# Performance work log

Hardware: AMD Instinct MI355X
Metric: run time of the kernel (lower is better)

The kernel has to match this reference:

```python
import jax, jax.numpy as jnp
import numpy as np

KS = 3
N = KS * KS
LN_EPS = 1e-5


def conv2d(x, w, stride=1, pad=0):
    return jax.lax.conv_general_dilated(
        x, w, (stride, stride), [(pad, pad), (pad, pad)],
        dimension_numbers=('NCHW', 'OIHW', 'NCHW'))


def layer_norm(x, g, b):
    mu = jnp.mean(x, axis=-1, keepdims=True)
    var = jnp.mean(jnp.square(x - mu), axis=-1, keepdims=True)
    return (x - mu) * jax.lax.rsqrt(var + LN_EPS) * g + b


def l2norm(x):
    n = jnp.sqrt(jnp.sum(jnp.square(x), axis=-1, keepdims=True))
    return x / jnp.maximum(n, 1e-12)


def deform_conv(x, w_p, b_p, w_d):
    # canonical DeformConv2d (kernel 3, pad 1, stride 1, no modulation)
    B, C, H, W = x.shape
    off = conv2d(x, w_p, stride=1, pad=1) + b_p[None, :, None, None]  # [B,2N,H,W]
    xp = jnp.pad(x, ((0, 0), (0, 0), (1, 1), (1, 1)))
    Hp, Wp = H + 2, W + 2
    pn = jnp.stack(jnp.meshgrid(jnp.arange(-1, 2), jnp.arange(-1, 2), indexing='ij'), 0)
    pn = pn.reshape(2, N).astype(x.dtype)  # kernel offsets, row-major (dx,dy)
    p0x = jnp.arange(1, H + 1, dtype=x.dtype)
    p0y = jnp.arange(1, W + 1, dtype=x.dtype)
    # sampling coords, [B,H,W,N]
    px = off[:, :N].transpose(0, 2, 3, 1) + p0x[None, :, None, None] + pn[0][None, None, None, :]
    py = off[:, N:].transpose(0, 2, 3, 1) + p0y[None, None, :, None] + pn[1][None, None, None, :]
    fx = jnp.floor(px)
    fy = jnp.floor(py)
    qlx = jnp.clip(fx, 0, Hp - 1)
    qly = jnp.clip(fy, 0, Wp - 1)
    qrx = jnp.clip(fx + 1, 0, Hp - 1)
    qry = jnp.clip(fy + 1, 0, Wp - 1)
    pxc = jnp.clip(px, 0, Hp - 1)
    pyc = jnp.clip(py, 0, Wp - 1)
    g_lt = (1 + (qlx - pxc)) * (1 + (qly - pyc))
    g_rb = (1 - (qrx - pxc)) * (1 - (qry - pyc))
    g_lb = (1 + (qlx - pxc)) * (1 - (qry - pyc))
    g_rt = (1 - (qrx - pxc)) * (1 + (qly - pyc))
    xf = xp.reshape(B, C, Hp * Wp)

    def gat(ix, iy):
        idx = (ix.astype(jnp.int32) * Wp + iy.astype(jnp.int32)).reshape(B, 1, -1)
        g = jnp.take_along_axis(xf, jnp.broadcast_to(idx, (B, C, idx.shape[-1])), axis=2)
        return g.reshape(B, C, H, W, N)

    xo = (g_lt[:, None] * gat(qlx, qly) + g_rb[:, None] * gat(qrx, qry)
          + g_lb[:, None] * gat(qlx, qry) + g_rt[:, None] * gat(qrx, qly))
    # [B,C,H,W,N] -> [B,C,H*ks,W*ks] (row = h*ks+kr, col = w*ks+kc)
    xo = xo.reshape(B, C, H, W, KS, KS).transpose(0, 1, 2, 4, 3, 5).reshape(B, C, H * KS, W * KS)
    return conv2d(xo, w_d, stride=KS, pad=0)


def setup_inputs() -> dict:
    key = jax.random.key(0)
    ks = jax.random.split(key, 8)
    B, C, H, W, heads = 4, 192, 64, 64, 6
    hid = 4 * C
    return {
        'x': jax.random.normal(ks[0], (B, C, H, W), dtype=jnp.float32),
        'gamma1': jnp.ones((C,), jnp.float32),
        'beta1': jnp.zeros((C,), jnp.float32),
        'gamma2': jnp.ones((C,), jnp.float32),
        'beta2': jnp.zeros((C,), jnp.float32),
        'temperature': jnp.ones((heads, 1, 1), jnp.float32),
        'w_qkv': jax.random.normal(ks[1], (3 * C, C), jnp.float32) * 0.02,
        'w_proj': jax.random.normal(ks[2], (C, C), jnp.float32) * 0.02,
        'w_p': jax.random.normal(ks[3], (2 * N, C, KS, KS), jnp.float32) * 0.01,
        'b_p': jnp.zeros((2 * N,), jnp.float32),
        'w_d': jax.random.normal(ks[4], (C, C, KS, KS), jnp.float32) * 0.02,
        'w_fc1': jax.random.normal(ks[5], (C, hid), jnp.float32) * 0.02,
        'b_fc1': jnp.zeros((hid,), jnp.float32),
        'w_fc2': jax.random.normal(ks[6], (hid, C), jnp.float32) * 0.02,
        'b_fc2': jnp.zeros((C,), jnp.float32),
    }


def reference(x, gamma1, beta1, gamma2, beta2, temperature, w_qkv, w_proj,
              w_p, b_p, w_d, w_fc1, b_fc1, w_fc2, b_fc2):
    B, C, H, W = x.shape
    heads = temperature.shape[0]
    xs = x.reshape(B, C, H * W).transpose(0, 2, 1)  # [B,HW,C]
    shortcut = xs
    xn = layer_norm(xs, gamma1, beta1).transpose(0, 2, 1).reshape(B, C, H, W)
    # SSA: deformable-conv query + channel attention over C
    q = deform_conv(xn, w_p, b_p, w_d)
    qkv = jnp.einsum('bchw,oc->bohw', xn, w_qkv)
    k_spe, v_spe = qkv[:, C:2 * C], qkv[:, 2 * C:]

    def split(t):
        return t.reshape(B, heads, C // heads, H * W)

    qh = split(q)
    kh = l2norm(split(k_spe))
    vh = l2norm(split(v_spe))
    attn = jnp.einsum('bhcn,bhdn->bhcd', qh, kh) * temperature[None]
    attn = jax.nn.softmax(attn, axis=-1)
    out = jnp.einsum('bhcd,bhdn->bhcn', attn, vh).reshape(B, C, H, W)
    out = jnp.einsum('bchw,oc->bohw', out, w_proj)
    xs2 = shortcut + out.reshape(B, C, H * W).transpose(0, 2, 1)
    h1 = layer_norm(xs2, gamma2, beta2)
    m = jax.nn.gelu(h1 @ w_fc1 + b_fc1, approximate=False) @ w_fc2 + b_fc2
    xs3 = xs2 + m
    return xs3.transpose(0, 2, 1).reshape(B, C, H, W)
```

## Files before the change

### kernel.cpp

```cpp
#include <hip/hip_runtime.h>
#include <math.h>

typedef unsigned short u16;
typedef unsigned int u32;
typedef short s16x8 __attribute__((ext_vector_type(8)));
typedef float f32x4 __attribute__((ext_vector_type(4)));

#define AS1 __attribute__((address_space(1)))
#define AS3 __attribute__((address_space(3)))

__device__ __forceinline__ float bf2f(u16 u) {
    union { u32 i; float f; } v; v.i = ((u32)u) << 16; return v.f;
}
__device__ __forceinline__ u16 f2bf(float f) {
    union { float f; u32 i; } v; v.f = f;
    u32 r = v.i + 0x7fffu + ((v.i >> 16) & 1u);
    return (u16)(r >> 16);
}
__device__ __forceinline__ void gll16(const u16* g, u16* l) {
    __builtin_amdgcn_global_load_lds((const AS1 u32*)g, (AS3 u32*)l, 16, 0, 0);
}

__global__ void prep_kernel(const float* __restrict__ wd, const float* __restrict__ wqkv,
                            const float* __restrict__ wfc1, const float* __restrict__ wfc2,
                            const float* __restrict__ wp,
                            u16* __restrict__ wdT, u16* __restrict__ wkvT,
                            u16* __restrict__ wf1T, u16* __restrict__ wf2T,
                            u16* __restrict__ wpT)
{
    int i = blockIdx.x * 256 + threadIdx.x;
    if (i < 331776) {
        int o = i / 1728, r = i % 1728;
        int p = r / 192, c = r % 192;
        int cs = c ^ ((o & 7) << 3);
        wdT[(p * 192 + o) * 192 + cs] = f2bf(wd[(o * 192 + c) * 9 + p]);
    }
    if (i < 73728) {
        int o = i / 192, c = i % 192;
        wkvT[i] = f2bf(wqkv[(192 + o) * 192 + c]);
    }
    if (i < 147456) {
        int n = i / 192, c = i % 192;
        wf1T[i] = f2bf(wfc1[c * 768 + n]);
        int n2 = i / 768, hh = i % 768;
        wf2T[i] = f2bf(wfc2[hh * 192 + n2]);
    }
    if (i < 31104) {
        int n = i / 1728, r = i % 1728;
        int p = r / 192, c = r % 192;
        wpT[i] = f2bf(wp[(n * 192 + c) * 9 + p]);
    } else if (i < 55296) {
        wpT[i] = 0;
    }
}

__global__ __launch_bounds__(256) void ln1_kernel(const float* __restrict__ x,
                                                  const float* __restrict__ g,
                                                  const float* __restrict__ be,
                                                  u16* __restrict__ xn)
{
    __shared__ float red0[256], red1[256];
    __shared__ float mu_s[64], rs_s[64];
    __shared__ float xt[64 * 193];
    __shared__ u16 tile[64 * 194];
    int t = threadIdx.x, tl = t & 63, cg = t >> 6;
    int m0 = blockIdx.x * 64;
    int b = m0 >> 12, hw0 = m0 & 4095;
    const float* xb = x + (size_t)b * 786432 + hw0 + tl;
    float s = 0.f, s2 = 0.f;
    for (int cc = cg; cc < 192; cc += 4) {
        float v = xb[cc * 4096];
        xt[tl * 193 + cc] = v;
        s += v; s2 += v * v;
    }
    red0[t] = s; red1[t] = s2;
    __syncthreads();
    if (t < 64) {
        float a = red0[t] + red0[64 + t] + red0[128 + t] + red0[192 + t];
        float q = red1[t] + red1[64 + t] + red1[128 + t] + red1[192 + t];
        float mu = a * (1.f / 192.f);
        float var = q * (1.f / 192.f) - mu * mu;
        mu_s[t] = mu; rs_s[t] = rsqrtf(var + 1e-5f);
    }
    __syncthreads();
    float mu = mu_s[tl], rs = rs_s[tl];
    for (int cc = cg; cc < 192; cc += 4) {
        float v = (xt[tl * 193 + cc] - mu) * rs * g[cc] + be[cc];
        tile[tl * 194 + cc] = f2bf(v);
    }
    __syncthreads();
    u32* dst = (u32*)(xn + (size_t)m0 * 192);
    for (int i = t; i < 64 * 96; i += 256) {
        int r = i / 96, c2 = i % 96;
        dst[i] = *(const u32*)&tile[r * 194 + c2 * 2];
    }
}

__global__ __launch_bounds__(256) void offconv_kernel(const u16* __restrict__ xn,
                                                      const u16* __restrict__ wpT,
                                                      const float* __restrict__ bp,
                                                      float* __restrict__ off)
{
    __shared__ u16 As[64 * 200];
    __shared__ u16 Bs[32 * 200];
    int bh = blockIdx.x;
    int b = bh >> 6, h = bh & 63;
    int t = threadIdx.x;
    int lane = t & 63, wv = t >> 6;
    f32x4 acc[2];
#pragma unroll
    for (int j = 0; j < 2; j++) { acc[j][0] = 0.f; acc[j][1] = 0.f; acc[j][2] = 0.f; acc[j][3] = 0.f; }
    int r = t >> 2, cq = (t & 3) * 48;
    for (int p = 0; p < 9; p++) {
        int dh = p / 3 - 1, dw = p % 3 - 1;
        int hr = h + dh, wr = r + dw;
        bool valid = (hr >= 0) && (hr < 64) && (wr >= 0) && (wr < 64);
        const u16* src = xn + ((size_t)(b * 4096 + hr * 64 + wr)) * 192 + cq;
#pragma unroll
        for (int j = 0; j < 6; j++) {
            s16x8 v = {0, 0, 0, 0, 0, 0, 0, 0};
            if (valid) v = *(const s16x8*)(src + j * 8);
            *(s16x8*)&As[r * 200 + cq + j * 8] = v;
        }
#pragma unroll
        for (int i = 0; i < 3; i++) {
            int q = t + i * 256;
            int n = q / 24, c8 = q % 24;
            *(s16x8*)&Bs[n * 200 + c8 * 8] =
                *(const s16x8*)(wpT + n * 1728 + p * 192 + c8 * 8);
        }
        __syncthreads();
#pragma unroll
        for (int kc = 0; kc < 6; kc++) {
            s16x8 af = *(const s16x8*)&As[(wv * 16 + (lane & 15)) * 200 + kc * 32 + (lane >> 4) * 8];
            s16x8 b0 = *(const s16x8*)&Bs[(lane & 15) * 200 + kc * 32 + (lane >> 4) * 8];
            s16x8 b1 = *(const s16x8*)&Bs[(16 + (lane & 15)) * 200 + kc * 32 + (lane >> 4) * 8];
            acc[0] = __builtin_amdgcn_mfma_f32_16x16x32_bf16(af, b0, acc[0], 0, 0, 0);
            acc[1] = __builtin_amdgcn_mfma_f32_16x16x32_bf16(af, b1, acc[1], 0, 0, 0);
        }
        __syncthreads();
    }
    int col = lane & 15;
    int wbase = wv * 16 + (lane >> 4) * 4;
#pragma unroll
    for (int j = 0; j < 2; j++) {
        int n = j * 16 + col;
        if (n < 18) {
            float bb = bp[n];
#pragma unroll
            for (int rr = 0; rr < 4; rr++) {
                int w = wbase + rr;
                off[((size_t)(b * 4096 + h * 64 + w)) * 18 + n] = acc[j][rr] + bb;
            }
        }
    }
}

__global__ __launch_bounds__(512, 2) void gemm_deform(const u16* __restrict__ xn,
                                                      const float* __restrict__ off,
                                                      const u16* __restrict__ wdT,
                                                      u16* __restrict__ qt)
{
    __shared__ u16 As[64 * 200];
    __shared__ u16 Bs[192 * 192];
    __shared__ int sidx[64][9][4];
    __shared__ float swt[64][9][4];
    int t = threadIdx.x, lane = t & 63, wv = t >> 6;
    int wm = wv & 1, wn = wv >> 1;
    int m0 = blockIdx.x * 64;
    int b = m0 >> 12;
    for (int i = t; i < 576; i += 512) {
        int mi = i / 9, p = i % 9;
        int m = m0 + mi;
        int hw = m & 4095;
        int h = hw >> 6, w = hw & 63;
        float ox = off[(size_t)m * 18 + p];
        float oy = off[(size_t)m * 18 + 9 + p];
        float px = ox + (float)(h + 1) + (float)(p / 3 - 1);
        float py = oy + (float)(w + 1) + (float)(p % 3 - 1);
        float fx = floorf(px), fy = floorf(py);
        float qlx = fminf(fmaxf(fx, 0.f), 65.f);
        float qly = fminf(fmaxf(fy, 0.f), 65.f);
        float qrx = fminf(fmaxf(fx + 1.f, 0.f), 65.f);
        float qry = fminf(fmaxf(fy + 1.f, 0.f), 65.f);
        float pxc = fminf(fmaxf(px, 0.f), 65.f);
        float pyc = fminf(fmaxf(py, 0.f), 65.f);
        float gxl = 1.f + (qlx - pxc), gxr = 1.f - (qrx - pxc);
        float gyl = 1.f + (qly - pyc), gyr = 1.f - (qry - pyc);
        int xl = (int)qlx, xr = (int)qrx, yl = (int)qly, yr = (int)qry;
        int cx[4] = {xl, xr, xl, xr};
        int cy[4] = {yl, yr, yr, yl};
        float cw[4] = {gxl * gyl, gxr * gyr, gxl * gyr, gxr * gyl};
#pragma unroll
        for (int k = 0; k < 4; k++) {
            bool ok = (cx[k] >= 1) && (cx[k] <= 64) && (cy[k] >= 1) && (cy[k] <= 64);
            sidx[mi][p][k] = ok ? (b * 4096 + (cx[k] - 1) * 64 + (cy[k] - 1)) * 192 : 0;
            swt[mi][p][k] = ok ? cw[k] : 0.f;
        }
    }
    __syncthreads();
    f32x4 acc[2][3];
#pragma unroll
    for (int i = 0; i < 2; i++)
#pragma unroll
        for (int j = 0; j < 3; j++) {
            acc[i][j][0] = 0.f; acc[i][j][1] = 0.f; acc[i][j][2] = 0.f; acc[i][j][3] = 0.f;
        }
    int mi = t >> 3, ch = (t & 7) * 24;
    int orow[3], oxr[3];
#pragma unroll
    for (int j = 0; j < 3; j++) {
        int o = wn * 48 + j * 16 + (lane & 15);
        orow[j] = o * 192;
        oxr[j] = (o & 7) << 3;
    }
    int kb0 = (lane >> 4) * 8;

    {
        const u16* bsrc = wdT;
#pragma unroll
        for (int i2 = 0; i2 < 9; i2++) {
            int jc = wv + 8 * i2;
            gll16(bsrc + jc * 512 + lane * 8, Bs + jc * 512);
        }
        const int*   si = sidx[mi][0];
        const float* sw = swt[mi][0];
        s16x8 pc[4][3];
#pragma unroll
        for (int k = 0; k < 4; k++)
#pragma unroll
            for (int s = 0; s < 3; s++)
                pc[k][s] = *(const s16x8*)(xn + si[k] + ch + s * 8);
        float v[24];
#pragma unroll
        for (int j = 0; j < 24; j++) v[j] = 0.f;
#pragma unroll
        for (int k = 0; k < 4; k++) {
            float wt = sw[k];
#pragma unroll
            for (int j = 0; j < 24; j++) v[j] += wt * bf2f((u16)pc[k][j >> 3][j & 7]);
        }
#pragma unroll
        for (int s = 0; s < 3; s++) {
            s16x8 ov;
#pragma unroll
            for (int e = 0; e < 8; e++) ov[e] = (short)f2bf(v[s * 8 + e]);
            *(s16x8*)&As[mi * 200 + ch + s * 8] = ov;
        }
        asm volatile("s_waitcnt vmcnt(0)" ::: "memory");
        __syncthreads();
    }

    for (int p = 0; p < 9; p++) {
        s16x8 nc[4][3];
        if (p < 8) {
            const int* si = sidx[mi][p + 1];
#pragma unroll
            for (int k = 0; k < 4; k++)
#pragma unroll
                for (int s = 0; s < 3; s++)
                    nc[k][s] = *(const s16x8*)(xn + si[k] + ch + s * 8);
        }
#pragma unroll
        for (int kk = 0; kk < 6; kk++) {
            int kb = kk * 32 + kb0;
            s16x8 af[2], bfr[3];
#pragma unroll
            for (int i = 0; i < 2; i++)
                af[i] = *(const s16x8*)&As[(wm * 32 + i * 16 + (lane & 15)) * 200 + kb];
#pragma unroll
            for (int j = 0; j < 3; j++)
                bfr[j] = *(const s16x8*)&Bs[orow[j] + (kb ^ oxr[j])];
#pragma unroll
            for (int i = 0; i < 2; i++)
#pragma unroll
                for (int j = 0; j < 3; j++)
                    acc[i][j] = __builtin_amdgcn_mfma_f32_16x16x32_bf16(af[i], bfr[j], acc[i][j], 0, 0, 0);
        }
        if (p < 8) {
            __syncthreads();
            const u16* bsrc = wdT + (size_t)(p + 1) * 36864;
#pragma unroll
            for (int i2 = 0; i2 < 9; i2++) {
                int jc = wv + 8 * i2;
                gll16(bsrc + jc * 512 + lane * 8, Bs + jc * 512);
            }
            const float* sw = swt[mi][p + 1];
            float v[24];
#pragma unroll
            for (int j = 0; j < 24; j++) v[j] = 0.f;
#pragma unroll
            for (int k = 0; k < 4; k++) {
                float wt = sw[k];
#pragma unroll
                for (int j = 0; j < 24; j++) v[j] += wt * bf2f((u16)nc[k][j >> 3][j & 7]);
            }
#pragma unroll
            for (int s = 0; s < 3; s++) {
                s16x8 ov;
#pragma unroll
                for (int e = 0; e < 8; e++) ov[e] = (short)f2bf(v[s * 8 + e]);
                *(s16x8*)&As[mi * 200 + ch + s * 8] = ov;
            }
            asm volatile("s_waitcnt vmcnt(0)" ::: "memory");
            __syncthreads();
        }
    }
    int col = lane & 15;
#pragma unroll
    for (int i = 0; i < 2; i++)
#pragma unroll
        for (int j = 0; j < 3; j++) {
            int mm = m0 + wm * 32 + i * 16 + (lane >> 4) * 4;
            int nn = wn * 48 + j * 16 + col;
#pragma unroll
            for (int r = 0; r < 4; r++)
                qt[(size_t)(mm + r) * 192 + nn] = f2bf(acc[i][j][r]);
        }
}

template<int BM, int BN, int WM, int WN, int EP>
__global__ __launch_bounds__((BM / WM) * (BN / WN) * 64)
void gemm_bt(const u16* __restrict__ A, int lda,
             const u16* __restrict__ B, int ldb, int bstride,
             void* __restrict__ out, int ldc,
             const float* __restrict__ ex1, int K,
             const float* __restrict__ ex2,
             const float* __restrict__ exg, const float* __restrict__ exb,
             void* __restrict__ out2)
{
    constexpr int BK = 32;
    constexpr int WAVES_M = BM / WM, WAVES_N = BN / WN, NW = WAVES_M * WAVES_N;
    constexpr int TM = WM / 16, TN = WN / 16;
    constexpr int NLA = BM / 16, NLB = BN / 16;
    __shared__ u16 As[BM * BK];
    __shared__ u16 Bs[BN * BK];
    int tid = threadIdx.x;
    int lane = tid & 63, wv = tid >> 6;
    int wm = wv % WAVES_M, wn = wv / WAVES_M;
    int m0 = blockIdx.x * BM, n0 = blockIdx.y * BN;
    const u16* Bp = B + (size_t)(m0 >> 12) * bstride;
    f32x4 acc[TM][TN];
#pragma unroll
    for (int i = 0; i < TM; i++)
#pragma unroll
        for (int j = 0; j < TN; j++) {
            acc[i][j][0] = 0.f; acc[i][j][1] = 0.f; acc[i][j][2] = 0.f; acc[i][j][3] = 0.f;
        }
    int arow_l = lane >> 2;
    int acol_l = (lane & 3) * 8;
    for (int k0 = 0; k0 < K; k0 += BK) {
#pragma unroll 1
        for (int j = wv; j < NLA + NLB; j += NW) {
            if (j < NLA) {
                int row = j * 16 + arow_l;
                gll16(A + (size_t)(m0 + row) * lda + k0 + acol_l, As + j * 512);
            } else {
                int row = (j - NLA) * 16 + arow_l;
                gll16(Bp + (size_t)(n0 + row) * ldb + k0 + acol_l, Bs + (j - NLA) * 512);
            }
        }
        asm volatile("s_waitcnt vmcnt(0)" ::: "memory");
        __syncthreads();
        s16x8 af[TM], bfr[TN];
#pragma unroll
        for (int i = 0; i < TM; i++)
            af[i] = *(const s16x8*)&As[(wm * WM + i * 16 + (lane & 15)) * BK + (lane >> 4) * 8];
#pragma unroll
        for (int j = 0; j < TN; j++)
            bfr[j] = *(const s16x8*)&Bs[(wn * WN + j * 16 + (lane & 15)) * BK + (lane >> 4) * 8];
#pragma unroll
        for (int i = 0; i < TM; i++)
#pragma unroll
            for (int j = 0; j < TN; j++)
                acc[i][j] = __builtin_amdgcn_mfma_f32_16x16x32_bf16(af[i], bfr[j], acc[i][j], 0, 0, 0);
        __syncthreads();
    }
    int col = lane & 15;
    int rg = lane >> 4;
    if constexpr (EP == 0) {
        u16* o = (u16*)out;
#pragma unroll
        for (int i = 0; i < TM; i++)
#pragma unroll
            for (int j = 0; j < TN; j++) {
                int mm = m0 + wm * WM + i * 16 + rg * 4;
                int nn = n0 + wn * WN + j * 16 + col;
#pragma unroll
                for (int r = 0; r < 4; r++) o[(size_t)(mm + r) * ldc + nn] = f2bf(acc[i][j][r]);
            }
    } else if constexpr (EP == 2) {
        u16* o = (u16*)out;
#pragma unroll
        for (int i = 0; i < TM; i++)
#pragma unroll
            for (int j = 0; j < TN; j++) {
                int mm = m0 + wm * WM + i * 16 + rg * 4;
                int nn = n0 + wn * WN + j * 16 + col;
                float bb = ex1[nn];
#pragma unroll
                for (int r = 0; r < 4; r++) {
                    float v = acc[i][j][r] + bb;
                    o[(size_t)(mm + r) * ldc + nn] = f2bf(0.5f * v * (1.f + erff(v * 0.70710678118654752f)));
                }
            }
    } else if constexpr (EP == 4) {
        __shared__ float lnA[BM][2];
        __shared__ float lnB[BM][2];
        float v[TM][TN][4];
        float sr[TM][4], sq[TM][4];
#pragma unroll
        for (int i = 0; i < TM; i++)
#pragma unroll
            for (int r = 0; r < 4; r++) { sr[i][r] = 0.f; sq[i][r] = 0.f; }
#pragma unroll
        for (int i = 0; i < TM; i++) {
            int mm = m0 + wm * WM + i * 16 + rg * 4;
#pragma unroll
            for (int j = 0; j < TN; j++) {
                int nn = n0 + wn * WN + j * 16 + col;
                const float* xr = ex1 + (size_t)(mm >> 12) * 786432 + (size_t)nn * 4096 + (mm & 4095);
#pragma unroll
                for (int r = 0; r < 4; r++) {
                    float vv = acc[i][j][r] + xr[r];
                    v[i][j][r] = vv;
                    sr[i][r] += vv; sq[i][r] += vv * vv;
                }
            }
        }
#pragma unroll
        for (int i = 0; i < TM; i++)
#pragma unroll
            for (int r = 0; r < 4; r++)
#pragma unroll
                for (int sh = 1; sh < 16; sh <<= 1) {
                    sr[i][r] += __shfl_xor(sr[i][r], sh);
                    sq[i][r] += __shfl_xor(sq[i][r], sh);
                }
        if (col == 0) {
#pragma unroll
            for (int i = 0; i < TM; i++)
#pragma unroll
                for (int r = 0; r < 4; r++) {
                    int row = wm * WM + i * 16 + rg * 4 + r;
                    lnA[row][wn] = sr[i][r];
                    lnB[row][wn] = sq[i][r];
                }
        }
        __syncthreads();
        float* oxs = (float*)out;
        u16* oh = (u16*)out2;
#pragma unroll
        for (int i = 0; i < TM; i++) {
            int mm = m0 + wm * WM + i * 16 + rg * 4;
#pragma unroll
            for (int r = 0; r < 4; r++) {
                int row = wm * WM + i * 16 + rg * 4 + r;
                float tot = lnA[row][0] + lnA[row][1];
                float tq  = lnB[row][0] + lnB[row][1];
                float mu = tot * (1.f / 192.f);
                float var = tq * (1.f / 192.f) - mu * mu;
                float rstd = rsqrtf(var + 1e-5f);
#pragma unroll
                for (int j = 0; j < TN; j++) {
                    int nn = n0 + wn * WN + j * 16 + col;
                    float vv = v[i][j][r];
                    oxs[(size_t)(mm + r) * ldc + nn] = vv;
                    oh[(size_t)(mm + r) * ldc + nn] = f2bf((vv - mu) * rstd * exg[nn] + exb[nn]);
                }
            }
        }
    } else if constexpr (EP == 5) {
        float* o = (float*)out;
#pragma unroll
        for (int i = 0; i < TM; i++)
#pragma unroll
            for (int j = 0; j < TN; j++) {
                int mm = m0 + wm * WM + i * 16 + rg * 4;
                int nn = n0 + wn * WN + j * 16 + col;
                float bb = ex1[nn];
                size_t obase = (size_t)(mm >> 12) * 786432 + (size_t)nn * 4096;
#pragma unroll
                for (int r = 0; r < 4; r++) {
                    float vv = acc[i][j][r] + bb + ex2[(size_t)(mm + r) * ldc + nn];
                    o[obase + ((mm + r) & 4095)] = vv;
                }
            }
    } else if constexpr (EP == 6) {
        u16* o = (u16*)out;
        float* nrm = (float*)out2;
        int bI = m0 >> 12;
#pragma unroll
        for (int j = 0; j < TN; j++) {
            float s = 0.f;
#pragma unroll
            for (int i = 0; i < TM; i++) {
                int mm = m0 + wm * WM + i * 16 + rg * 4;
                int nn = n0 + wn * WN + j * 16 + col;
#pragma unroll
                for (int r = 0; r < 4; r++) {
                    u16 hb = f2bf(acc[i][j][r]);
                    o[(size_t)(mm + r) * ldc + nn] = hb;
                    float fv = bf2f(hb);
                    s += fv * fv;
                }
            }
            s += __shfl_xor(s, 16);
            s += __shfl_xor(s, 32);
            if (rg == 0) {
                int nn = n0 + wn * WN + j * 16 + col;
                atomicAdd(&nrm[bI * 384 + nn], s);
            }
        }
    }
}

__global__ __launch_bounds__(64) void attnp_kernel(const u16* __restrict__ qt,
                                                   const u16* __restrict__ kvt,
                                                   float* __restrict__ raw)
{
    __shared__ float qT[32 * 69];
    __shared__ float kT[32 * 69];
    int ch = blockIdx.x, h = blockIdx.y, b = blockIdx.z;
    int t = threadIdx.x;
    size_t base = (size_t)(b * 4096 + ch * 64);
    for (int e = t; e < 2048; e += 64) {
        int r = e >> 5, c = e & 31;
        qT[c * 69 + r] = bf2f(qt[(base + r) * 192 + h * 32 + c]);
        kT[c * 69 + r] = bf2f(kvt[(base + r) * 384 + h * 32 + c]);
    }
    __syncthreads();
    int tc = t >> 3, td = t & 7;
    int c0 = tc * 4, d0 = td * 4;
    float acc[4][4] = {};
    for (int r = 0; r < 64; r++) {
        float qv[4], kv4[4];
#pragma unroll
        for (int u = 0; u < 4; u++) { qv[u] = qT[(c0 + u) * 69 + r]; kv4[u] = kT[(d0 + u) * 69 + r]; }
#pragma unroll
        for (int u = 0; u < 4; u++)
#pragma unroll
            for (int v = 0; v < 4; v++) acc[u][v] += qv[u] * kv4[v];
    }
    float* dst = raw + (((size_t)(b * 6 + h) * 64 + ch) * 1024);
#pragma unroll
    for (int u = 0; u < 4; u++)
#pragma unroll
        for (int v = 0; v < 4; v++)
            dst[(c0 + u) * 32 + d0 + v] = acc[u][v];
}

__global__ __launch_bounds__(1024) void softmax_kernel(const float* __restrict__ raw,
                                                       const float* __restrict__ norm2,
                                                       const float* __restrict__ temp,
                                                       float* __restrict__ att2)
{
    int h = blockIdx.x, b = blockIdx.y;
    int t = threadIdx.x;
    int c = t >> 5, d = t & 31;
    __shared__ float invk[32], invv[32];
    if (t < 32)       invk[t] = 1.f / fmaxf(sqrtf(norm2[b * 384 + h * 32 + t]), 1e-12f);
    else if (t < 64)  invv[t - 32] = 1.f / fmaxf(sqrtf(norm2[b * 384 + 192 + h * 32 + (t - 32)]), 1e-12f);
    __syncthreads();
    float T = temp[h];
    const float* pr = raw + (size_t)(b * 6 + h) * 65536 + c * 32 + d;
    float v = 0.f;
#pragma unroll
    for (int ch = 0; ch < 64; ch++) v += pr[ch * 1024];
    v *= invk[d] * T;
    float mx = v;
    for (int s = 16; s > 0; s >>= 1) mx = fmaxf(mx, __shfl_xor(mx, s, 32));
    float e = expf(v - mx);
    float sm = e;
    for (int s = 16; s > 0; s >>= 1) sm += __shfl_xor(sm, s, 32);
    att2[((size_t)(b * 6 + h) * 32 + c) * 32 + d] = (e / sm) * invv[d];
}

__global__ __launch_bounds__(192) void mb_kernel(const float* __restrict__ wproj,
                                                 const float* __restrict__ att2,
                                                 u16* __restrict__ Mb)
{
    int o2 = blockIdx.x, b = blockIdx.y, t = threadIdx.x;
    int h = t >> 5, d = t & 31;
    float s = 0.f;
#pragma unroll
    for (int c = 0; c < 32; c++)
        s += wproj[o2 * 192 + h * 32 + c] * att2[((size_t)(b * 6 + h) * 32 + c) * 32 + d];
    Mb[((size_t)b * 192 + o2) * 192 + t] = f2bf(s);
}

extern "C" void kernel_launch(void* const* d_in, const int* in_sizes, int n_in,
                              void* d_out, int out_size, void* d_ws, size_t ws_size,
                              hipStream_t stream)
{
    const float* x      = (const float*)d_in[0];
    const float* gamma1 = (const float*)d_in[1];
    const float* beta1  = (const float*)d_in[2];
    const float* gamma2 = (const float*)d_in[3];
    const float* beta2  = (const float*)d_in[4];
    const float* temp   = (const float*)d_in[5];
    const float* w_qkv  = (const float*)d_in[6];
    const float* w_proj = (const float*)d_in[7];
    const float* w_p    = (const float*)d_in[8];
    const float* b_p    = (const float*)d_in[9];
    const float* w_d    = (const float*)d_in[10];
    const float* w_fc1  = (const float*)d_in[11];
    const float* b_fc1  = (const float*)d_in[12];
    const float* w_fc2  = (const float*)d_in[13];
    const float* b_fc2  = (const float*)d_in[14];
    float* out = (float*)d_out;
    char* ws = (char*)d_ws;

    u16*   xn    = (u16*)(ws + 0);
    float* off   = (float*)(ws + 6291456);
    u16*   adef  = (u16*)(ws + 7471104);
    u16*   wpT   = adef;
    u16*   m1    = adef;
    float* araw  = (float*)(ws + 32636928);
    u16*   qt    = (u16*)(ws + 64094208);
    u16*   kvt   = (u16*)(ws + 70385664);
    float* norm2 = (float*)(ws + 82968576);
    float* att2  = (float*)(ws + 83073024);
    u16*   Mb    = (u16*)(ws + 83171328);
    float* xs2   = (float*)(ws + 83318784);
    u16*   h1    = xn;
    u16*   wdT   = (u16*)(ws + 95901696);
    u16*   wkvT  = (u16*)(ws + 96565248);
    u16*   wf1T  = (u16*)(ws + 96712704);
    u16*   wf2T  = (u16*)(ws + 97007616);

    hipMemsetAsync(norm2, 0, 6144, stream);
    prep_kernel<<<1296, 256, 0, stream>>>(w_d, w_qkv, w_fc1, w_fc2, w_p, wdT, wkvT, wf1T, wf2T, wpT);
    ln1_kernel<<<256, 256, 0, stream>>>(x, gamma1, beta1, xn);
    offconv_kernel<<<256, 256, 0, stream>>>(xn, wpT, b_p, off);
    gemm_deform<<<256, 512, 0, stream>>>(xn, off, wdT, qt);
    gemm_bt<128, 128, 64, 64, 6><<<dim3(128, 3), 256, 0, stream>>>(
        xn, 192, wkvT, 192, 0, kvt, 384, nullptr, 192, nullptr, nullptr, nullptr, norm2);
    attnp_kernel<<<dim3(64, 6, 4), 64, 0, stream>>>(qt, kvt, araw);
    softmax_kernel<<<dim3(6, 4), 1024, 0, stream>>>(araw, norm2, temp, att2);
    mb_kernel<<<dim3(192, 4), 192, 0, stream>>>(w_proj, att2, Mb);
    gemm_bt<64, 192, 32, 96, 4><<<dim3(256, 1), 256, 0, stream>>>(
        kvt + 192, 384, Mb, 192, 192 * 192, xs2, 192, x, 192, nullptr, gamma2, beta2, h1);
    gemm_bt<128, 128, 64, 64, 2><<<dim3(128, 6), 256, 0, stream>>>(
        h1, 192, wf1T, 192, 0, m1, 768, b_fc1, 192, nullptr, nullptr, nullptr, nullptr);
    gemm_bt<128, 96, 64, 48, 5><<<dim3(128, 2), 256, 0, stream>>>(
        m1, 768, wf2T, 768, 0, out, 192, b_fc2, 768, xs2, nullptr, nullptr, nullptr);
}
```

Baseline: 244.3 us.

## Fuse both MLP GEMMs into one kernel keeping the GELU hidden layer in LDS

Replaces the separate fc1 (with GELU epilogue) and fc2 (with bias and residual epilogue) GEMM launches with a single mlp_kernel. Each 64-row block computes the full 768-wide hidden activation, stores it as bf16 in shared memory, then runs the second GEMM from LDS. This removes the global write and re-read of the hidden tensor and one kernel launch. In exchange it uses only 256 blocks with large LDS and one block per CU, and B operands are read straight from global memory without LDS staging, which may lower occupancy and hurt latency hiding.

```diff
diff --git a/kernel.cpp b/kernel.cpp
--- a/kernel.cpp
+++ b/kernel.cpp
@@ -325,7 +325,6 @@
              const u16* __restrict__ B, int ldb, int bstride,
              void* __restrict__ out, int ldc,
              const float* __restrict__ ex1, int K,
-             const float* __restrict__ ex2,
              const float* __restrict__ exg, const float* __restrict__ exb,
              void* __restrict__ out2)
 {
@@ -378,33 +377,7 @@
     }
     int col = lane & 15;
     int rg = lane >> 4;
-    if constexpr (EP == 0) {
-        u16* o = (u16*)out;
-#pragma unroll
-        for (int i = 0; i < TM; i++)
-#pragma unroll
-            for (int j = 0; j < TN; j++) {
-                int mm = m0 + wm * WM + i * 16 + rg * 4;
-                int nn = n0 + wn * WN + j * 16 + col;
-#pragma unroll
-                for (int r = 0; r < 4; r++) o[(size_t)(mm + r) * ldc + nn] = f2bf(acc[i][j][r]);
-            }
-    } else if constexpr (EP == 2) {
-        u16* o = (u16*)out;
-#pragma unroll
-        for (int i = 0; i < TM; i++)
-#pragma unroll
-            for (int j = 0; j < TN; j++) {
-                int mm = m0 + wm * WM + i * 16 + rg * 4;
-                int nn = n0 + wn * WN + j * 16 + col;
-                float bb = ex1[nn];
-#pragma unroll
-                for (int r = 0; r < 4; r++) {
-                    float v = acc[i][j][r] + bb;
-                    o[(size_t)(mm + r) * ldc + nn] = f2bf(0.5f * v * (1.f + erff(v * 0.70710678118654752f)));
-                }
-            }
-    } else if constexpr (EP == 4) {
+    if constexpr (EP == 4) {
         __shared__ float lnA[BM][2];
         __shared__ float lnB[BM][2];
         float v[TM][TN][4];
@@ -470,22 +443,6 @@
                 }
             }
         }
-    } else if constexpr (EP == 5) {
-        float* o = (float*)out;
-#pragma unroll
-        for (int i = 0; i < TM; i++)
-#pragma unroll
-            for (int j = 0; j < TN; j++) {
-                int mm = m0 + wm * WM + i * 16 + rg * 4;
-                int nn = n0 + wn * WN + j * 16 + col;
-                float bb = ex1[nn];
-                size_t obase = (size_t)(mm >> 12) * 786432 + (size_t)nn * 4096;
-#pragma unroll
-                for (int r = 0; r < 4; r++) {
-                    float vv = acc[i][j][r] + bb + ex2[(size_t)(mm + r) * ldc + nn];
-                    o[obase + ((mm + r) & 4095)] = vv;
-                }
-            }
     } else if constexpr (EP == 6) {
         u16* o = (u16*)out;
         float* nrm = (float*)out2;
@@ -513,6 +470,98 @@
             }
         }
     }
+}
+
+__global__ __launch_bounds__(512, 1) void mlp_kernel(const u16* __restrict__ h1,
+                                                     const u16* __restrict__ wf1T,
+                                                     const u16* __restrict__ wf2T,
+                                                     const float* __restrict__ b1,
+                                                     const float* __restrict__ b2,
+                                                     const float* __restrict__ xs2,
+                                                     float* __restrict__ out)
+{
+    __shared__ u16 As[64 * 32];
+    __shared__ u16 m1s[64][776];
+    int t = threadIdx.x, lane = t & 63, wv = t >> 6;
+    int wm = wv & 1, wn = wv >> 1;
+    int m0 = blockIdx.x * 64;
+    int col = lane & 15, rg = lane >> 4;
+    int arow = lane >> 2, acol = (lane & 3) * 8;
+
+    f32x4 acc[2][12];
+#pragma unroll
+    for (int i = 0; i < 2; i++)
+#pragma unroll
+        for (int j = 0; j < 12; j++) {
+            acc[i][j][0] = 0.f; acc[i][j][1] = 0.f; acc[i][j][2] = 0.f; acc[i][j][3] = 0.f;
+        }
+    for (int k = 0; k < 6; k++) {
+        if (wv < 4)
+            gll16(h1 + (size_t)(m0 + wv * 16 + arow) * 192 + k * 32 + acol, As + wv * 512);
+        asm volatile("s_waitcnt vmcnt(0)" ::: "memory");
+        __syncthreads();
+        s16x8 af[2];
+#pragma unroll
+        for (int i = 0; i < 2; i++)
+            af[i] = *(const s16x8*)&As[(wm * 32 + i * 16 + (lane & 15)) * 32 + rg * 8];
+#pragma unroll
+        for (int j = 0; j < 12; j++) {
+            s16x8 bfr = *(const s16x8*)(wf1T + (size_t)(wn * 192 + j * 16 + (lane & 15)) * 192 + k * 32 + rg * 8);
+#pragma unroll
+            for (int i = 0; i < 2; i++)
+                acc[i][j] = __builtin_amdgcn_mfma_f32_16x16x32_bf16(af[i], bfr, acc[i][j], 0, 0, 0);
+        }
+        __syncthreads();
+    }
+#pragma unroll
+    for (int i = 0; i < 2; i++)
+#pragma unroll
+        for (int j = 0; j < 12; j++) {
+            int row = wm * 32 + i * 16 + rg * 4;
+            int nn = wn * 192 + j * 16 + col;
+            float bb = b1[nn];
+#pragma unroll
+            for (int r = 0; r < 4; r++) {
+                float v = acc[i][j][r] + bb;
+                m1s[row + r][nn] = f2bf(0.5f * v * (1.f + erff(v * 0.70710678118654752f)));
+            }
+        }
+    __syncthreads();
+
+    f32x4 a2[2][3];
+#pragma unroll
+    for (int i = 0; i < 2; i++)
+#pragma unroll
+        for (int j = 0; j < 3; j++) {
+            a2[i][j][0] = 0.f; a2[i][j][1] = 0.f; a2[i][j][2] = 0.f; a2[i][j][3] = 0.f;
+        }
+    for (int kk = 0; kk < 24; kk++) {
+        s16x8 af[2];
+#pragma unroll
+        for (int i = 0; i < 2; i++)
+            af[i] = *(const s16x8*)&m1s[wm * 32 + i * 16 + (lane & 15)][kk * 32 + rg * 8];
+#pragma unroll
+        for (int j = 0; j < 3; j++) {
+            s16x8 bfr = *(const s16x8*)(wf2T + (size_t)(wn * 48 + j * 16 + (lane & 15)) * 768 + kk * 32 + rg * 8);
+#pragma unroll
+            for (int i = 0; i < 2; i++)
+                a2[i][j] = __builtin_amdgcn_mfma_f32_16x16x32_bf16(af[i], bfr, a2[i][j], 0, 0, 0);
+        }
+    }
+#pragma unroll
+    for (int i = 0; i < 2; i++)
+#pragma unroll
+        for (int j = 0; j < 3; j++) {
+            int mm = m0 + wm * 32 + i * 16 + rg * 4;
+            int nn = wn * 48 + j * 16 + col;
+            float bb = b2[nn];
+            size_t obase = (size_t)(mm >> 12) * 786432 + (size_t)nn * 4096;
+#pragma unroll
+            for (int r = 0; r < 4; r++) {
+                float vv = a2[i][j][r] + bb + xs2[(size_t)(mm + r) * 192 + nn];
+                out[obase + ((mm + r) & 4095)] = vv;
+            }
+        }
 }
 
 __global__ __launch_bounds__(64) void attnp_kernel(const u16* __restrict__ qt,
@@ -613,9 +662,7 @@
 
     u16*   xn    = (u16*)(ws + 0);
     float* off   = (float*)(ws + 6291456);
-    u16*   adef  = (u16*)(ws + 7471104);
-    u16*   wpT   = adef;
-    u16*   m1    = adef;
+    u16*   wpT   = (u16*)(ws + 7471104);
     float* araw  = (float*)(ws + 32636928);
     u16*   qt    = (u16*)(ws + 64094208);
     u16*   kvt   = (u16*)(ws + 70385664);
@@ -635,14 +682,11 @@
     offconv_kernel<<<256, 256, 0, stream>>>(xn, wpT, b_p, off);
     gemm_deform<<<256, 512, 0, stream>>>(xn, off, wdT, qt);
     gemm_bt<128, 128, 64, 64, 6><<<dim3(128, 3), 256, 0, stream>>>(
-        xn, 192, wkvT, 192, 0, kvt, 384, nullptr, 192, nullptr, nullptr, nullptr, norm2);
+        xn, 192, wkvT, 192, 0, kvt, 384, nullptr, 192, nullptr, nullptr, norm2);
     attnp_kernel<<<dim3(64, 6, 4), 64, 0, stream>>>(qt, kvt, araw);
     softmax_kernel<<<dim3(6, 4), 1024, 0, stream>>>(araw, norm2, temp, att2);
     mb_kernel<<<dim3(192, 4), 192, 0, stream>>>(w_proj, att2, Mb);
     gemm_bt<64, 192, 32, 96, 4><<<dim3(256, 1), 256, 0, stream>>>(
-        kvt + 192, 384, Mb, 192, 192 * 192, xs2, 192, x, 192, nullptr, gamma2, beta2, h1);
-    gemm_bt<128, 128, 64, 64, 2><<<dim3(128, 6), 256, 0, stream>>>(
-        h1, 192, wf1T, 192, 0, m1, 768, b_fc1, 192, nullptr, nullptr, nullptr, nullptr);
-    gemm_bt<128, 96, 64, 48, 5><<<dim3(128, 2), 256, 0, stream>>>(
-        m1, 768, wf2T, 768, 0, out, 192, b_fc2, 768, xs2, nullptr, nullptr, nullptr);
-}
+        kvt + 192, 384, Mb, 192, 192 * 192, xs2, 192, x, 192, gamma2, beta2, h1);
+    mlp_kernel<<<256, 512, 0, stream>>>(h1, wf1T, wf2T, b_fc1, b_fc2, xs2, out);
+}
```

Result: slower. 252.3 us (+3.3%).
